# Kernel tuning notes

Hardware: AMD Instinct MI355X
Metric: run time of the kernel (lower is better)

Reference implementation:

```python
import jax, jax.numpy as jnp
import numpy as np

B, T, V, NNZ = 4, 2048, 32000, 801
TAU, RARE, ALPHA = 0.8, 1.0, 0.7


def setup_inputs() -> dict:
    key = jax.random.key(0)
    k1, k2, k3, k4, k5 = jax.random.split(key, 5)
    logp = jax.nn.log_softmax(jax.random.normal(k1, (B, T, V), jnp.float32), axis=-1)
    target = jax.random.randint(k2, (B, T), 0, V, dtype=jnp.int32)
    mask = jnp.ones((B, T), jnp.float32)
    sim_values = jax.random.uniform(k3, (V, NNZ), jnp.float32)  # raw similarities in [0,1]
    idf_values = jax.random.uniform(k4, (V, NNZ), jnp.float32)
    sim_cols = jax.random.randint(k5, (V, NNZ), 0, V, dtype=jnp.int32)
    return {"logp": logp, "mask": mask, "sim_values": sim_values,
            "idf_values": idf_values, "target": target, "sim_cols": sim_cols}


def reference(logp, mask, sim_values, idf_values, target, sim_cols):
    N = B * T
    lp = logp.reshape(N, V)          # [N, V]
    rows = target.reshape(N)         # [N]
    m = mask.reshape(N)              # [N]

    # get_submatrix: per-target-row slice of the fixed-nnz sparse sim matrix
    vals = sim_values[rows] - 1.0 - TAU * RARE * idf_values[rows]  # [N, NNZ]
    # faithful to original: exp applied twice (exp(exp(v/tau)/tau))
    vals = jnp.exp(jnp.exp(vals / TAU) / TAU)
    sim = vals / jnp.sum(vals, axis=1, keepdims=True)              # row-normalized

    cols = sim_cols[rows]                                          # [N, NNZ]
    g = jnp.take_along_axis(lp, cols, axis=1)                      # gathered logp

    denom = jnp.sum(m)
    smooth_loss = -jnp.sum(g * sim) / denom                        # smoothed NLL
    ml_loss = -jnp.sum(jnp.take_along_axis(lp, rows[:, None], axis=1)[:, 0] * m) / denom
    return ALPHA * smooth_loss + (1.0 - ALPHA) * ml_loss
```

## Files before the change

kernel.cpp:

```cpp
#include <hip/hip_runtime.h>

#define VOCAB 32000
#define NNZ   801
#define NNZ_FULL 768
#define NNZ_TAIL 33
#define NROWS 8192
#define ROWS_PER_BLOCK 4

__device__ __forceinline__ float warp_reduce_add_f(float v) {
    #pragma unroll
    for (int off = 32; off > 0; off >>= 1) v += __shfl_down(v, off, 64);
    return v;
}

__global__ __launch_bounds__(256) void wordsmooth_main(
        const float* __restrict__ logp,
        const float* __restrict__ mask,
        const float* __restrict__ sim_values,
        const float* __restrict__ idf_values,
        const int*   __restrict__ target,
        const int*   __restrict__ sim_cols,
        double*      __restrict__ partials)
{
    const int lane = threadIdx.x & 63;
    const int wave = threadIdx.x >> 6;
    const int row  = blockIdx.x * ROWS_PER_BLOCK + wave;
    if (row >= NROWS) return;

    const int trow = target[row];
    const float* __restrict__ lp_row = logp + (size_t)row * VOCAB;
    const float* __restrict__ sv_p = sim_values + (size_t)trow * NNZ;
    const float* __restrict__ iv_p = idf_values + (size_t)trow * NNZ;
    const int*   __restrict__ sc_p = sim_cols   + (size_t)trow * NNZ;

    const float TAU_INV  = 1.25f;
    const float TAU_RARE = 0.8f;

    float s_v = 0.0f, s_gv = 0.0f;

    #pragma unroll 4
    for (int j = lane; j < NNZ_FULL; j += 64) {
        float sv = __builtin_nontemporal_load(sv_p + j);
        float iv = __builtin_nontemporal_load(iv_p + j);
        int   c  = __builtin_nontemporal_load(sc_p + j);
        float x   = (sv - 1.0f - TAU_RARE * iv) * TAU_INV;
        float val = __expf(__expf(x) * TAU_INV);
        float g   = lp_row[c];
        s_v  += val;
        s_gv += g * val;
    }
    if (lane < NNZ_TAIL) {
        int j = NNZ_FULL + lane;
        float sv = __builtin_nontemporal_load(sv_p + j);
        float iv = __builtin_nontemporal_load(iv_p + j);
        int   c  = __builtin_nontemporal_load(sc_p + j);
        float x   = (sv - 1.0f - TAU_RARE * iv) * TAU_INV;
        float val = __expf(__expf(x) * TAU_INV);
        float g   = lp_row[c];
        s_v  += val;
        s_gv += g * val;
    }

    s_v  = warp_reduce_add_f(s_v);
    s_gv = warp_reduce_add_f(s_gv);

    if (lane == 0) {
        float m = mask[row];
        partials[row]             = (double)(-s_gv / s_v);
        partials[NROWS + row]     = (double)(-lp_row[trow] * m);
        partials[2 * NROWS + row] = (double)m;
    }
}

__global__ __launch_bounds__(256) void wordsmooth_finalize(
        const double* __restrict__ partials, float* __restrict__ out)
{
    double s = 0.0, ml = 0.0, dn = 0.0;
    for (int i = threadIdx.x; i < NROWS; i += 256) {
        s  += partials[i];
        ml += partials[NROWS + i];
        dn += partials[2 * NROWS + i];
    }
    #pragma unroll
    for (int off = 32; off > 0; off >>= 1) {
        s  += __shfl_down(s,  off, 64);
        ml += __shfl_down(ml, off, 64);
        dn += __shfl_down(dn, off, 64);
    }
    __shared__ double sh[3][4];
    const int lane = threadIdx.x & 63;
    const int wave = threadIdx.x >> 6;
    if (lane == 0) { sh[0][wave] = s; sh[1][wave] = ml; sh[2][wave] = dn; }
    __syncthreads();
    if (threadIdx.x == 0) {
        double S = 0.0, M = 0.0, D = 0.0;
        #pragma unroll
        for (int w = 0; w < 4; ++w) { S += sh[0][w]; M += sh[1][w]; D += sh[2][w]; }
        const double ALPHA = 0.7;
        out[0] = (float)((ALPHA * S + (1.0 - ALPHA) * M) / D);
    }
}

extern "C" void kernel_launch(void* const* d_in, const int* in_sizes, int n_in,
                              void* d_out, int out_size, void* d_ws, size_t ws_size,
                              hipStream_t stream) {
    const float* logp       = (const float*)d_in[0];
    const float* mask       = (const float*)d_in[1];
    const float* sim_values = (const float*)d_in[2];
    const float* idf_values = (const float*)d_in[3];
    const int*   target     = (const int*)d_in[4];
    const int*   sim_cols   = (const int*)d_in[5];
    float* out = (float*)d_out;
    double* partials = (double*)d_ws;

    dim3 grid(NROWS / ROWS_PER_BLOCK);
    dim3 block(256);
    wordsmooth_main<<<grid, block, 0, stream>>>(logp, mask, sim_values, idf_values,
                                                target, sim_cols, partials);
    wordsmooth_finalize<<<1, 256, 0, stream>>>(partials, out);
}
```

Baseline: 1.354 ms.

## Stream logp rows into LDS via global_load_lds and gather from shared memory

Each output row now gets two 512-thread blocks, one per half of the vocabulary. Each block copies its half of the logp row (16384 floats) into LDS with async global_load_lds, then does the 801 sparse gathers from LDS. The idea is to replace latency-bound random global gathers with contiguous streaming reads. This reads the whole logp tensor rather than only the touched cache lines, and 64KB of LDS per block limits occupancy. The partials layout and finalize kernel are reworked to combine the per-half gv and ml sums and compute the per-row normalization there.

```diff
diff --git a/kernel.cpp b/kernel.cpp
--- a/kernel.cpp
+++ b/kernel.cpp
@@ -2,18 +2,28 @@
 
 #define VOCAB 32000
 #define NNZ   801
-#define NNZ_FULL 768
-#define NNZ_TAIL 33
 #define NROWS 8192
-#define ROWS_PER_BLOCK 4
+#define THREADS 512
 
-__device__ __forceinline__ float warp_reduce_add_f(float v) {
+#define HALF_FLOATS 16384
+#define HALF1_BASE  (VOCAB - HALF_FLOATS)
+#define SPLIT       16000
+
+#define GV_OFF 0
+#define SV_OFF (2*NROWS)
+#define ML_OFF (3*NROWS)
+#define MV_OFF (5*NROWS)
+
+typedef const __attribute__((address_space(1))) unsigned int* gaddr_t;
+typedef __attribute__((address_space(3))) unsigned int* laddr_t;
+
+__device__ __forceinline__ float wave_reduce_add_f(float v) {
     #pragma unroll
     for (int off = 32; off > 0; off >>= 1) v += __shfl_down(v, off, 64);
     return v;
 }
 
-__global__ __launch_bounds__(256) void wordsmooth_main(
+__global__ __launch_bounds__(THREADS) void wordsmooth_main(
         const float* __restrict__ logp,
         const float* __restrict__ mask,
         const float* __restrict__ sim_values,
@@ -22,75 +32,102 @@
         const int*   __restrict__ sim_cols,
         double*      __restrict__ partials)
 {
-    const int lane = threadIdx.x & 63;
-    const int wave = threadIdx.x >> 6;
-    const int row  = blockIdx.x * ROWS_PER_BLOCK + wave;
-    if (row >= NROWS) return;
+    __shared__ float lds[HALF_FLOATS];
+
+    const int tid  = threadIdx.x;
+    const int lane = tid & 63;
+    const int wave = tid >> 6;
+    const int row  = blockIdx.x >> 1;
+    const int half = blockIdx.x & 1;
+    const int base = half ? HALF1_BASE : 0;
 
     const int trow = target[row];
-    const float* __restrict__ lp_row = logp + (size_t)row * VOCAB;
     const float* __restrict__ sv_p = sim_values + (size_t)trow * NNZ;
     const float* __restrict__ iv_p = idf_values + (size_t)trow * NNZ;
     const int*   __restrict__ sc_p = sim_cols   + (size_t)trow * NNZ;
+    const float* __restrict__ grow = logp + (size_t)row * VOCAB + base;
 
     const float TAU_INV  = 1.25f;
     const float TAU_RARE = 0.8f;
 
-    float s_v = 0.0f, s_gv = 0.0f;
+    float sv0 = sv_p[tid];
+    float iv0 = iv_p[tid];
+    int   c0  = sc_p[tid];
+    const bool has1 = (tid < (NNZ - THREADS));
+    float sv1 = 0.0f, iv1 = 0.0f; int c1 = 0;
+    if (has1) { sv1 = sv_p[tid + THREADS]; iv1 = iv_p[tid + THREADS]; c1 = sc_p[tid + THREADS]; }
 
-    #pragma unroll 4
-    for (int j = lane; j < NNZ_FULL; j += 64) {
-        float sv = __builtin_nontemporal_load(sv_p + j);
-        float iv = __builtin_nontemporal_load(iv_p + j);
-        int   c  = __builtin_nontemporal_load(sc_p + j);
-        float x   = (sv - 1.0f - TAU_RARE * iv) * TAU_INV;
-        float val = __expf(__expf(x) * TAU_INV);
-        float g   = lp_row[c];
-        s_v  += val;
-        s_gv += g * val;
-    }
-    if (lane < NNZ_TAIL) {
-        int j = NNZ_FULL + lane;
-        float sv = __builtin_nontemporal_load(sv_p + j);
-        float iv = __builtin_nontemporal_load(iv_p + j);
-        int   c  = __builtin_nontemporal_load(sc_p + j);
-        float x   = (sv - 1.0f - TAU_RARE * iv) * TAU_INV;
-        float val = __expf(__expf(x) * TAU_INV);
-        float g   = lp_row[c];
-        s_v  += val;
-        s_gv += g * val;
+    #pragma unroll
+    for (int r = 0; r < 8; ++r) {
+        const int foff = wave * 2048 + r * 256;
+        __builtin_amdgcn_global_load_lds(
+            (gaddr_t)(grow + foff + lane * 4),
+            (laddr_t)(lds + foff), 16, 0, 0);
     }
 
-    s_v  = warp_reduce_add_f(s_v);
-    s_gv = warp_reduce_add_f(s_gv);
+    float x0 = (sv0 - 1.0f - TAU_RARE * iv0) * TAU_INV;
+    float v0 = __expf(__expf(x0) * TAU_INV);
+    float v1 = 0.0f;
+    if (has1) {
+        float x1 = (sv1 - 1.0f - TAU_RARE * iv1) * TAU_INV;
+        v1 = __expf(__expf(x1) * TAU_INV);
+    }
+    float s_v = v0 + v1;
 
-    if (lane == 0) {
-        float m = mask[row];
-        partials[row]             = (double)(-s_gv / s_v);
-        partials[NROWS + row]     = (double)(-lp_row[trow] * m);
-        partials[2 * NROWS + row] = (double)m;
+    __syncthreads();
+
+    float s_gv = 0.0f;
+    const bool mine0 = half ? (c0 >= SPLIT) : (c0 < SPLIT);
+    if (mine0) s_gv += v0 * lds[c0 - base];
+    if (has1) {
+        const bool mine1 = half ? (c1 >= SPLIT) : (c1 < SPLIT);
+        if (mine1) s_gv += v1 * lds[c1 - base];
+    }
+
+    float lp_t = 0.0f;
+    const bool own_ml = half ? (trow >= SPLIT) : (trow < SPLIT);
+    if (tid == 0 && own_ml) lp_t = lds[trow - base];
+
+    s_v  = wave_reduce_add_f(s_v);
+    s_gv = wave_reduce_add_f(s_gv);
+    __syncthreads();
+    if (lane == 0) { lds[wave] = s_gv; lds[8 + wave] = s_v; }
+    __syncthreads();
+    if (tid == 0) {
+        float gv = 0.0f, vv = 0.0f;
+        #pragma unroll
+        for (int w = 0; w < 8; ++w) { gv += lds[w]; vv += lds[8 + w]; }
+        const float m = mask[row];
+        partials[GV_OFF + 2 * row + half] = (double)gv;
+        partials[ML_OFF + 2 * row + half] = own_ml ? (double)(-lp_t * m) : 0.0;
+        if (!half) {
+            partials[SV_OFF + row] = (double)vv;
+            partials[MV_OFF + row] = (double)m;
+        }
     }
 }
 
 __global__ __launch_bounds__(256) void wordsmooth_finalize(
         const double* __restrict__ partials, float* __restrict__ out)
 {
-    double s = 0.0, ml = 0.0, dn = 0.0;
-    for (int i = threadIdx.x; i < NROWS; i += 256) {
-        s  += partials[i];
-        ml += partials[NROWS + i];
-        dn += partials[2 * NROWS + i];
+    double sm = 0.0, ml = 0.0, dn = 0.0;
+    for (int r = threadIdx.x; r < NROWS; r += 256) {
+        double gv = partials[GV_OFF + 2 * r] + partials[GV_OFF + 2 * r + 1];
+        double sv = partials[SV_OFF + r];
+        sm += -gv / sv;
+        ml += partials[ML_OFF + 2 * r] + partials[ML_OFF + 2 * r + 1];
+        dn += partials[MV_OFF + r];
     }
     #pragma unroll
     for (int off = 32; off > 0; off >>= 1) {
-        s  += __shfl_down(s,  off, 64);
+        sm += __shfl_down(sm, off, 64);
         ml += __shfl_down(ml, off, 64);
         dn += __shfl_down(dn, off, 64);
     }
     __shared__ double sh[3][4];
     const int lane = threadIdx.x & 63;
     const int wave = threadIdx.x >> 6;
-    if (lane == 0) { sh[0][wave] = s; sh[1][wave] = ml; sh[2][wave] = dn; }
+    if (lane == 0) { sh[0][wave] = sm; sh[1][wave] = ml; sh[2][wave] = dn; }
     __syncthreads();
     if (threadIdx.x == 0) {
         double S = 0.0, M = 0.0, D = 0.0;
@@ -113,8 +150,8 @@
     float* out = (float*)d_out;
     double* partials = (double*)d_ws;
 
-    dim3 grid(NROWS / ROWS_PER_BLOCK);
-    dim3 block(256);
+    dim3 grid(2 * NROWS);
+    dim3 block(THREADS);
     wordsmooth_main<<<grid, block, 0, stream>>>(logp, mask, sim_values, idf_values,
                                                 target, sim_cols, partials);
     wordsmooth_finalize<<<1, 256, 0, stream>>>(partials, out);
```

After: 1.431 ms. +5.6%, slower.
